# Kernel tuning notes

Measured on AMD Instinct MI355X. Metric: run time of the kernel, lower is better.

Reference implementation:

```python
import jax, jax.numpy as jnp
import numpy as np

NUM_HEADS = 16
D_MODEL = 1024
D_K = D_MODEL // NUM_HEADS
EPS = 1e-6


def setup_inputs() -> dict:
    key = jax.random.key(0)
    ks = jax.random.split(key, 12)
    B, S, D = 8, 1024, D_MODEL
    scale = 0.02
    return {
        "query": jax.random.normal(ks[0], (B, S, D), dtype=jnp.float32),
        "key": jax.random.normal(ks[1], (B, S, D), dtype=jnp.float32),
        "value": jax.random.normal(ks[2], (B, S, D), dtype=jnp.float32),
        "policy": jax.random.uniform(ks[3], (B, S, 1), dtype=jnp.float32),
        "wq_w": jax.random.normal(ks[4], (D, D), dtype=jnp.float32) * scale,
        "wq_b": jnp.zeros((D,), dtype=jnp.float32),
        "wk_w": jax.random.normal(ks[5], (D, D), dtype=jnp.float32) * scale,
        "wk_b": jnp.zeros((D,), dtype=jnp.float32),
        "wv_w": jax.random.normal(ks[6], (D, D), dtype=jnp.float32) * scale,
        "wv_b": jnp.zeros((D,), dtype=jnp.float32),
        "dense_w": jax.random.normal(ks[7], (D, D), dtype=jnp.float32) * scale,
        "dense_b": jnp.zeros((D,), dtype=jnp.float32),
    }


def _split_heads(x):
    B, S, D = x.shape
    return x.reshape(B, S, NUM_HEADS, D_K).transpose(0, 2, 1, 3)  # [B,H,S,dk]


def reference(query, key, value, policy, wq_w, wq_b, wk_w, wk_b, wv_w, wv_b, dense_w, dense_b):
    B, S, D = query.shape
    # torch Linear: y = x @ W.T + b
    q = _split_heads(query @ wq_w.T + wq_b)
    k = _split_heads(key @ wk_w.T + wk_b)
    v = _split_heads(value @ wv_w.T + wv_b)

    scores = jnp.einsum("bhqd,bhkd->bhqk", q, k) / jnp.sqrt(jnp.float32(D_K))
    # policy branch: exp * policy normalization (no softmax max-subtraction, faithful)
    attn_policy = policy.reshape(B, 1, 1, S)
    sc = jnp.exp(scores) * attn_policy
    p_attn = (sc + EPS / S) / (jnp.sum(sc, axis=-1, keepdims=True) + EPS)

    x = jnp.einsum("bhqk,bhkd->bhqd", p_attn, v)
    x = x.transpose(0, 2, 1, 3).reshape(B, S, D)
    out = x @ dense_w.T + dense_b  # dropout = identity (eval mode)
    return out
```

## Files before the change

kernel.cpp:

```cpp
#include <hip/hip_runtime.h>


#define Sdim 1024
#define Ddim 1024

typedef unsigned short u16;
typedef float f32x4 __attribute__((ext_vector_type(4)));
typedef float f32x16 __attribute__((ext_vector_type(16)));
typedef __bf16 bf16x8 __attribute__((ext_vector_type(8)));
typedef u16 u16x8 __attribute__((ext_vector_type(8)));
typedef unsigned u32x2 __attribute__((ext_vector_type(2)));
typedef __attribute__((address_space(3))) void lds_void;
typedef __attribute__((address_space(1))) void gbl_void;

__device__ __forceinline__ u16 f2bf(float f) {
    unsigned u = __float_as_uint(f);
    u += 0x7fffu + ((u >> 16) & 1u);
    return (u16)(u >> 16);
}
__device__ __forceinline__ void gld16(const void* g, void* l) {
    __builtin_amdgcn_global_load_lds((const gbl_void*)g, (lds_void*)l, 16, 0, 0);
}
__device__ __forceinline__ float fexp2(float x) {
#if __has_builtin(__builtin_amdgcn_exp2f)
    return __builtin_amdgcn_exp2f(x);
#else
    return __expf(x * 0.6931471805599453f);
#endif
}
__device__ __forceinline__ unsigned cvtpk(float lo, float hi) {
    unsigned r;
    asm("v_cvt_pk_bf16_f32 %0, %1, %2" : "=v"(r) : "v"(lo), "v"(hi));
    return r;
}
#define MFMA16(a, b, c) __builtin_amdgcn_mfma_f32_16x16x32_bf16((a), (b), (c), 0, 0, 0)
#define MFMA32(a, b, c) __builtin_amdgcn_mfma_f32_32x32x16_bf16((a), (b), (c), 0, 0, 0)
#define SCHEDB() __builtin_amdgcn_sched_barrier(0)

#define QSCALE 0.18033688011112042f

__global__ __launch_bounds__(256) void cvt_all(const float* __restrict__ s0,
                                               const float* __restrict__ s1,
                                               const float* __restrict__ s2,
                                               const float* __restrict__ s3,
                                               const float* __restrict__ s4,
                                               const float* __restrict__ s5,
                                               const float* __restrict__ s6,
                                               u16* __restrict__ d0, u16* __restrict__ d1,
                                               u16* __restrict__ d2, u16* __restrict__ d3,
                                               u16* __restrict__ d4, u16* __restrict__ d5,
                                               u16* __restrict__ d6) {
    const int z = blockIdx.y;
    if (z >= 3 && blockIdx.x >= 512) return;
    const float* s = z == 0 ? s0 : z == 1 ? s1 : z == 2 ? s2 : z == 3 ? s3
                   : z == 4 ? s4 : z == 5 ? s5 : s6;
    u16* d = z == 0 ? d0 : z == 1 ? d1 : z == 2 ? d2 : z == 3 ? d3
           : z == 4 ? d4 : z == 5 ? d5 : d6;
    const float sc = (z == 3) ? QSCALE : 1.0f;
    const int i = (blockIdx.x * 256 + threadIdx.x) * 8;
    const float4 a = *(const float4*)(s + i);
    const float4 b = *(const float4*)(s + i + 4);
    u16x8 o;
    o[0] = f2bf(a.x * sc); o[1] = f2bf(a.y * sc); o[2] = f2bf(a.z * sc); o[3] = f2bf(a.w * sc);
    o[4] = f2bf(b.x * sc); o[5] = f2bf(b.y * sc); o[6] = f2bf(b.z * sc); o[7] = f2bf(b.w * sc);
    *(u16x8*)(d + i) = o;
}

template <int OM>
__device__ __forceinline__ void gemm2p_body(const u16* __restrict__ A,
                                            const u16* __restrict__ W,
                                            const float* __restrict__ bias, float bscale,
                                            void* __restrict__ Cout,
                                            char* __restrict__ smem,
                                            int m0, int n0) {
    const int tid  = threadIdx.x;
    const int w    = tid >> 6;
    const int lane = tid & 63;
    const int l15  = lane & 15;
    const int quad = lane >> 4;
    const int wr   = w >> 1;
    const int wc   = w & 1;

    const int lrow = lane >> 3;
    const int scol = (((lane & 7) ^ lrow) << 3);
    const u16* pa = A + (size_t)(m0 + w * 32 + lrow) * Ddim + scol;
    const u16* pb = W + (size_t)(n0 + w * 16 + lrow) * Ddim + scol;
    char* sAw = smem + w * 4096;
    char* sBw = smem + 65536 + w * 2048;

#define STG(t, b)                                                             \
    do {                                                                      \
        const int k0 = (t) * 64;                                              \
        gld16(pa + k0,             sAw + (b) * 32768);                        \
        gld16(pa + k0 + 8 * 1024,  sAw + (b) * 32768 + 1024);                 \
        gld16(pa + k0 + 16 * 1024, sAw + (b) * 32768 + 2048);                 \
        gld16(pa + k0 + 24 * 1024, sAw + (b) * 32768 + 3072);                 \
        gld16(pb + k0,             sBw + (b) * 16384);                        \
        gld16(pb + k0 + 8 * 1024,  sBw + (b) * 16384 + 1024);                 \
    } while (0)

    const char* Ab = smem + (size_t)(wr * 64 + l15) * 128;
    const char* Bb = smem + 65536 + (size_t)(wc * 64 + l15) * 128;
    const int cx = ((quad ^ (l15 & 7)) << 4);

    f32x4 acc[4][4] = {};

    STG(0, 0);
    __syncthreads();

    for (int t = 0; t < 16; ++t) {
        const int boA = (t & 1) * 32768;
        const int boB = (t & 1) * 16384;
        if (t < 15) STG(t + 1, (t & 1) ^ 1);
        SCHEDB();
#pragma unroll
        for (int ks = 0; ks < 2; ++ks) {
            const int cxs = cx ^ (ks << 6);
            bf16x8 af[4], bfr[4];
#pragma unroll
            for (int i = 0; i < 4; ++i)
                af[i] = *(const bf16x8*)(Ab + boA + i * 2048 + cxs);
#pragma unroll
            for (int j = 0; j < 4; ++j)
                bfr[j] = *(const bf16x8*)(Bb + boB + j * 2048 + cxs);
#pragma unroll
            for (int i = 0; i < 4; ++i)
#pragma unroll
                for (int j = 0; j < 4; ++j)
                    acc[i][j] = MFMA16(af[i], bfr[j], acc[i][j]);
        }
        __syncthreads();
    }
#undef STG

    float bv[4];
#pragma unroll
    for (int j = 0; j < 4; ++j)
        bv[j] = bias[n0 + wc * 64 + j * 16 + l15] * bscale;

    if (OM == 2) {
        u16* Ts = (u16*)smem;
#pragma unroll
        for (int i = 0; i < 4; ++i)
#pragma unroll
            for (int j = 0; j < 4; ++j)
#pragma unroll
                for (int r = 0; r < 4; ++r)
                    Ts[(wr * 64 + i * 16 + quad * 4 + r) * 133 +
                       wc * 64 + j * 16 + l15] = f2bf(acc[i][j][r] + bv[j]);
        __syncthreads();
        const int dcol = tid >> 2;
        const int sp   = tid & 3;
        const int b    = m0 >> 10;
        const int sb0  = m0 & 1023;
        const int h    = (n0 >> 6) + (dcol >> 6);
        const int dd   = dcol & 63;
        u16* vrow = (u16*)Cout + ((size_t)((b << 4) + h) * 64 + dd) * Sdim + sb0;
#pragma unroll
        for (int sblk = 0; sblk < 4; ++sblk)
#pragma unroll
            for (int g = 0; g < 2; ++g) {
                const int c = sblk * 64 + sp * 16 + g * 8;
                u16x8 o;
#pragma unroll
                for (int e = 0; e < 8; ++e) o[e] = Ts[(c + e) * 133 + dcol];
                *(u16x8*)(vrow + c) = o;
            }
    } else {
#pragma unroll
        for (int i = 0; i < 4; ++i)
#pragma unroll
            for (int j = 0; j < 4; ++j)
#pragma unroll
                for (int r = 0; r < 4; ++r) {
                    const int row = m0 + wr * 64 + i * 16 + quad * 4 + r;
                    const int col = n0 + wc * 64 + j * 16 + l15;
                    const float v = acc[i][j][r] + bv[j];
                    if (OM == 1)
                        ((u16*)Cout)[(size_t)row * Ddim + col] = f2bf(v);
                    else
                        ((float*)Cout)[(size_t)row * Ddim + col] = v;
                }
    }
}

__global__ __launch_bounds__(512, 2) void gemm2p_qkv(
        const u16* __restrict__ A0, const u16* __restrict__ A1, const u16* __restrict__ A2,
        const u16* __restrict__ W0, const u16* __restrict__ W1, const u16* __restrict__ W2,
        const float* __restrict__ b0, const float* __restrict__ b1, const float* __restrict__ b2,
        u16* __restrict__ C0, u16* __restrict__ C1, u16* __restrict__ C2) {
    __shared__ __align__(16) char smem[98304];
    const int d = blockIdx.x;
    const int s = (d & 7) * 96 + (d >> 3);
    const int z = s >> 8;
    const int rr = s & 255;
    const int tm = rr >> 3, tn = rr & 7;
    const u16* A = z == 0 ? A0 : z == 1 ? A1 : A2;
    const u16* W = z == 0 ? W0 : z == 1 ? W1 : W2;
    const float* bias = z == 0 ? b0 : z == 1 ? b1 : b2;
    u16* C = z == 0 ? C0 : z == 1 ? C1 : C2;
    const float bsc = (z == 0) ? QSCALE : 1.0f;
    if (z == 2)
        gemm2p_body<2>(A, W, bias, bsc, (void*)C, smem, tm * 256, tn * 128);
    else
        gemm2p_body<1>(A, W, bias, bsc, (void*)C, smem, tm * 256, tn * 128);
}

__global__ __launch_bounds__(512, 2) void gemm2p_dense(const u16* __restrict__ A,
                                                       const u16* __restrict__ W,
                                                       const float* __restrict__ bias,
                                                       float* __restrict__ C) {
    __shared__ __align__(16) char smem[98304];
    const int d = blockIdx.x;
    const int s = (d & 7) * 32 + (d >> 3);
    const int tm = s >> 3, tn = s & 7;
    gemm2p_body<0>(A, W, bias, 1.0f, (void*)C, smem, tm * 256, tn * 128);
}

__global__ __launch_bounds__(256, 2) void attn_mfma(const u16* __restrict__ Qp,
                                                    const u16* __restrict__ Kp,
                                                    const u16* __restrict__ Vt,
                                                    const float* __restrict__ pol,
                                                    u16* __restrict__ Xb) {
    __shared__ __align__(16) u16 lds[37632];
    u16* Qs = lds;
    u16* Ks = lds + 18432;
    u16* Vs = lds + 27648;
    float* pols = (float*)(lds + 36864);
    float* denb = pols + 128;

    const int tid  = threadIdx.x;
    const int w    = tid >> 6;
    const int lane = tid & 63;
    const int l31  = lane & 31;
    const unsigned hsel = lane >> 5;
    const int bh = blockIdx.x;
    const int q0 = blockIdx.y * 256;
    const size_t bS = (size_t)(bh >> 4) * Sdim;
    const int col0 = (bh & 15) * 64;
    const int sr = tid >> 2;
    const int sc4 = tid & 3;

    const u16* Kg = Kp + (bS + sr) * Ddim + col0 + sc4 * 8;
    const u16* Vg = Vt + ((size_t)(bh * 64 + sr)) * Sdim + sc4 * 8;
    const float* pg = pol + bS + tid;

#pragma unroll
    for (int rg = 0; rg < 4; ++rg) {
        const int r = rg * 64 + sr;
#pragma unroll
        for (int g = 0; g < 2; ++g) {
            const int ch = sc4 + g * 4;
            *(u16x8*)(Qs + r * 72 + ch * 8) =
                *(const u16x8*)(Qp + (bS + q0 + r) * Ddim + col0 + ch * 8);
        }
    }
#pragma unroll
    for (int g = 0; g < 2; ++g) {
        *(u16x8*)(Ks + sr * 72 + (sc4 + g * 4) * 8) = *(const u16x8*)(Kg + g * 32);
        *(u16x8*)(Vs + sr * 72 + (sc4 + g * 4) * 8) = *(const u16x8*)(Vg + g * 32);
    }
    if (tid < 64) pols[tid] = pg[0];
    __syncthreads();

    bf16x8 Qf[2][4];
#pragma unroll
    for (int qt = 0; qt < 2; ++qt)
#pragma unroll
        for (int dkt = 0; dkt < 4; ++dkt)
            Qf[qt][dkt] = *(const bf16x8*)(Qs + (w * 64 + qt * 32 + l31) * 72 +
                                           dkt * 16 + hsel * 8);

    f32x16 X[2][2] = {};
    float den[2] = {0.f, 0.f};

    for (int kt = 0; kt < 16; ++kt) {
        const int cur = kt & 1;
        const bool pf = (kt < 15);
        u16x8 kr0 = {}, kr1 = {}, vr0 = {}, vr1 = {};
        float polr = 0.f;
        if (pf) {
            const int ko = (kt + 1) * 64;
            kr0 = *(const u16x8*)(Kg + (size_t)ko * Ddim);
            kr1 = *(const u16x8*)(Kg + (size_t)ko * Ddim + 32);
            vr0 = *(const u16x8*)(Vg + ko);
            vr1 = *(const u16x8*)(Vg + ko + 32);
            if (tid < 64) polr = pg[ko];
        }
        SCHEDB();

        const u16* Ksc = Ks + cur * 4608;
        const u16* Vsc = Vs + cur * 4608;
        const float* polc = pols + cur * 64;
#pragma unroll
        for (int t32 = 0; t32 < 2; ++t32) {
            float polv[16];
#pragma unroll
            for (int e = 0; e < 16; ++e)
                polv[e] = polc[t32 * 32 + (e & 3) + 8 * (e >> 2) + 4 * hsel];
            bf16x8 Kf[4];
#pragma unroll
            for (int dkt = 0; dkt < 4; ++dkt)
                Kf[dkt] = *(const bf16x8*)(Ksc + (t32 * 32 + l31) * 72 +
                                           dkt * 16 + hsel * 8);
#pragma unroll
            for (int qt = 0; qt < 2; ++qt) {
                f32x16 S = {};
#pragma unroll
                for (int dkt = 0; dkt < 4; ++dkt)
                    S = MFMA32(Kf[dkt], Qf[qt][dkt], S);
                float p[16];
#pragma unroll
                for (int e = 0; e < 16; ++e) {
                    p[e] = fexp2(S[e]) * polv[e];
                    den[qt] += p[e];
                }
                unsigned pk_[8];
#pragma unroll
                for (int g = 0; g < 4; ++g) {
                    pk_[2 * g]     = cvtpk(p[4 * g + 0], p[4 * g + 1]);
                    pk_[2 * g + 1] = cvtpk(p[4 * g + 2], p[4 * g + 3]);
                }
#pragma unroll
                for (int tau = 0; tau < 2; ++tau) {
                    const u32x2 sA = __builtin_amdgcn_permlane32_swap(
                        pk_[4 * tau + 0], pk_[4 * tau + 2], false, false);
                    const u32x2 sB = __builtin_amdgcn_permlane32_swap(
                        pk_[4 * tau + 1], pk_[4 * tau + 3], false, false);
                    union { unsigned u[4]; bf16x8 v; } Af;
                    Af.u[0] = sA[0]; Af.u[1] = sB[0];
                    Af.u[2] = sA[1]; Af.u[3] = sB[1];
#pragma unroll
                    for (int ndt = 0; ndt < 2; ++ndt) {
                        const bf16x8 Vf =
                            *(const bf16x8*)(Vsc + (ndt * 32 + l31) * 72 +
                                             t32 * 32 + tau * 16 + hsel * 8);
                        X[qt][ndt] = MFMA32(Af.v, Vf, X[qt][ndt]);
                    }
                }
            }
        }
        if (pf) {
            const int nxt = cur ^ 1;
            *(u16x8*)(Ks + nxt * 4608 + sr * 72 + sc4 * 8) = kr0;
            *(u16x8*)(Ks + nxt * 4608 + sr * 72 + (sc4 + 4) * 8) = kr1;
            *(u16x8*)(Vs + nxt * 4608 + sr * 72 + sc4 * 8) = vr0;
            *(u16x8*)(Vs + nxt * 4608 + sr * 72 + (sc4 + 4) * 8) = vr1;
            if (tid < 64) pols[nxt * 64 + tid] = polr;
        }
        __syncthreads();
    }

#pragma unroll
    for (int qt = 0; qt < 2; ++qt) {
        den[qt] += __shfl_xor(den[qt], 32);
        denb[w * 64 + qt * 32 + l31] = 1.0f / (den[qt] + 1e-6f);
    }
    u16* Xout = Qs;
#pragma unroll
    for (int qt = 0; qt < 2; ++qt) {
        float invv[16];
#pragma unroll
        for (int e = 0; e < 16; ++e)
            invv[e] = denb[w * 64 + qt * 32 + (e & 3) + 8 * (e >> 2) + 4 * hsel];
#pragma unroll
        for (int ndt = 0; ndt < 2; ++ndt)
#pragma unroll
            for (int e = 0; e < 16; ++e) {
                const int rho = (e & 3) + 8 * (e >> 2) + 4 * hsel;
                Xout[(w * 64 + qt * 32 + rho) * 72 + ndt * 32 + l31] =
                    f2bf(X[qt][ndt][e] * invv[e]);
            }
    }
    __syncthreads();
#pragma unroll
    for (int rg = 0; rg < 4; ++rg) {
        const int r = rg * 64 + sr;
#pragma unroll
        for (int g = 0; g < 2; ++g) {
            const int ch = sc4 + g * 4;
            *(u16x8*)(Xb + (bS + q0 + r) * Ddim + col0 + ch * 8) =
                *(const u16x8*)(Xout + r * 72 + ch * 8);
        }
    }
}

extern "C" void kernel_launch(void* const* d_in, const int* in_sizes, int n_in,
                              void* d_out, int out_size, void* d_ws, size_t ws_size,
                              hipStream_t stream) {
    const float* query   = (const float*)d_in[0];
    const float* key     = (const float*)d_in[1];
    const float* value   = (const float*)d_in[2];
    const float* policy  = (const float*)d_in[3];
    const float* wq_w    = (const float*)d_in[4];
    const float* wq_b    = (const float*)d_in[5];
    const float* wk_w    = (const float*)d_in[6];
    const float* wk_b    = (const float*)d_in[7];
    const float* wv_w    = (const float*)d_in[8];
    const float* wv_b    = (const float*)d_in[9];
    const float* dense_w = (const float*)d_in[10];
    const float* dense_b = (const float*)d_in[11];

    const size_t MM = 1u << 20;
    const size_t A8 = 8 * MM;
    u16* qa  = (u16*)d_ws;
    u16* ka  = qa + A8;
    u16* va  = ka + A8;
    u16* wqb = va + A8;
    u16* wkb = wqb + MM;
    u16* wvb = wkb + MM;
    u16* wdb = wvb + MM;
    u16* Qp  = wdb + MM;
    u16* Kp  = Qp + A8;
    u16* Vt  = Kp + A8;
    u16* Xb  = qa;

    cvt_all<<<dim3(4096, 7), 256, 0, stream>>>(query, key, value, wq_w, wk_w, wv_w, dense_w,
                                               qa, ka, va, wqb, wkb, wvb, wdb);

    gemm2p_qkv<<<dim3(768), 512, 0, stream>>>(qa, ka, va, wqb, wkb, wvb,
                                              wq_b, wk_b, wv_b, Qp, Kp, Vt);

    attn_mfma<<<dim3(128, 4), 256, 0, stream>>>(Qp, Kp, Vt, policy, Xb);

    gemm2p_dense<<<dim3(256), 512, 0, stream>>>(Xb, wdb, dense_b, (float*)d_out);
}
```

Measured before the change: 292.3 us.

## Fuse fp32-to-bf16 activation conversion into QKV GEMM A-tile staging

Removes the separate conversion pass over query/key/value. The QKV GEMM now loads fp32 activations into registers, converts them to packed bf16 and writes them to LDS after the MFMA loop of each K-step, so the global loads overlap compute. The weights are still converted by a smaller kernel. This saves the write and re-read of the bf16 activation copies, at the cost of more register pressure and VALU/LDS-store work inside the GEMM. Each A element is now read from global memory at 4 bytes once per N-tile.

```diff
diff --git a/kernel.cpp b/kernel.cpp
--- a/kernel.cpp
+++ b/kernel.cpp
@@ -10,6 +10,7 @@
 typedef __bf16 bf16x8 __attribute__((ext_vector_type(8)));
 typedef u16 u16x8 __attribute__((ext_vector_type(8)));
 typedef unsigned u32x2 __attribute__((ext_vector_type(2)));
+typedef unsigned u32x4 __attribute__((ext_vector_type(4)));
 typedef __attribute__((address_space(3))) void lds_void;
 typedef __attribute__((address_space(1))) void gbl_void;
 
@@ -39,24 +40,16 @@
 
 #define QSCALE 0.18033688011112042f
 
-__global__ __launch_bounds__(256) void cvt_all(const float* __restrict__ s0,
-                                               const float* __restrict__ s1,
-                                               const float* __restrict__ s2,
-                                               const float* __restrict__ s3,
-                                               const float* __restrict__ s4,
-                                               const float* __restrict__ s5,
-                                               const float* __restrict__ s6,
-                                               u16* __restrict__ d0, u16* __restrict__ d1,
-                                               u16* __restrict__ d2, u16* __restrict__ d3,
-                                               u16* __restrict__ d4, u16* __restrict__ d5,
-                                               u16* __restrict__ d6) {
+__global__ __launch_bounds__(256) void cvt_w(const float* __restrict__ s0,
+                                             const float* __restrict__ s1,
+                                             const float* __restrict__ s2,
+                                             const float* __restrict__ s3,
+                                             u16* __restrict__ d0, u16* __restrict__ d1,
+                                             u16* __restrict__ d2, u16* __restrict__ d3) {
     const int z = blockIdx.y;
-    if (z >= 3 && blockIdx.x >= 512) return;
-    const float* s = z == 0 ? s0 : z == 1 ? s1 : z == 2 ? s2 : z == 3 ? s3
-                   : z == 4 ? s4 : z == 5 ? s5 : s6;
-    u16* d = z == 0 ? d0 : z == 1 ? d1 : z == 2 ? d2 : z == 3 ? d3
-           : z == 4 ? d4 : z == 5 ? d5 : d6;
-    const float sc = (z == 3) ? QSCALE : 1.0f;
+    const float* s = z == 0 ? s0 : z == 1 ? s1 : z == 2 ? s2 : s3;
+    u16* d = z == 0 ? d0 : z == 1 ? d1 : z == 2 ? d2 : d3;
+    const float sc = (z == 0) ? QSCALE : 1.0f;
     const int i = (blockIdx.x * 256 + threadIdx.x) * 8;
     const float4 a = *(const float4*)(s + i);
     const float4 b = *(const float4*)(s + i + 4);
@@ -66,8 +59,8 @@
     *(u16x8*)(d + i) = o;
 }
 
-template <int OM>
-__device__ __forceinline__ void gemm2p_body(const u16* __restrict__ A,
+template <int OM, bool AF32>
+__device__ __forceinline__ void gemm2p_body(const void* __restrict__ Asrc,
                                             const u16* __restrict__ W,
                                             const float* __restrict__ bias, float bscale,
                                             void* __restrict__ Cout,
@@ -83,20 +76,49 @@
 
     const int lrow = lane >> 3;
     const int scol = (((lane & 7) ^ lrow) << 3);
-    const u16* pa = A + (size_t)(m0 + w * 32 + lrow) * Ddim + scol;
+    const u16*   pa  = AF32 ? nullptr
+                            : (const u16*)Asrc + (size_t)(m0 + w * 32 + lrow) * Ddim + scol;
+    const float* paf = AF32 ? (const float*)Asrc + (size_t)(m0 + w * 32 + lrow) * Ddim + scol
+                            : nullptr;
     const u16* pb = W + (size_t)(n0 + w * 16 + lrow) * Ddim + scol;
     char* sAw = smem + w * 4096;
+    char* sAd = sAw + lane * 16;
     char* sBw = smem + 65536 + w * 2048;
 
-#define STG(t, b)                                                             \
+#define STG_A16(t, b)                                                         \
     do {                                                                      \
         const int k0 = (t) * 64;                                              \
         gld16(pa + k0,             sAw + (b) * 32768);                        \
         gld16(pa + k0 + 8 * 1024,  sAw + (b) * 32768 + 1024);                 \
         gld16(pa + k0 + 16 * 1024, sAw + (b) * 32768 + 2048);                 \
         gld16(pa + k0 + 24 * 1024, sAw + (b) * 32768 + 3072);                 \
-        gld16(pb + k0,             sBw + (b) * 16384);                        \
-        gld16(pb + k0 + 8 * 1024,  sBw + (b) * 16384 + 1024);                 \
+    } while (0)
+#define LDF(t, r0, r1)                                                        \
+    do {                                                                      \
+        const float* pt_ = paf + (t) * 64;                                    \
+        _Pragma("unroll")                                                     \
+        for (int j_ = 0; j_ < 4; ++j_) {                                      \
+            r0[j_] = *(const float4*)(pt_ + j_ * 8192);                       \
+            r1[j_] = *(const float4*)(pt_ + j_ * 8192 + 4);                   \
+        }                                                                     \
+    } while (0)
+#define WRF(b, r0, r1)                                                        \
+    do {                                                                      \
+        _Pragma("unroll")                                                     \
+        for (int j_ = 0; j_ < 4; ++j_) {                                      \
+            u32x4 o_;                                                         \
+            o_[0] = cvtpk(r0[j_].x, r0[j_].y);                                \
+            o_[1] = cvtpk(r0[j_].z, r0[j_].w);                                \
+            o_[2] = cvtpk(r1[j_].x, r1[j_].y);                                \
+            o_[3] = cvtpk(r1[j_].z, r1[j_].w);                                \
+            *(u32x4*)(sAd + (b) * 32768 + j_ * 1024) = o_;                    \
+        }                                                                     \
+    } while (0)
+#define STG_B(t, b)                                                           \
+    do {                                                                      \
+        const int k0 = (t) * 64;                                              \
+        gld16(pb + k0,            sBw + (b) * 16384);                         \
+        gld16(pb + k0 + 8 * 1024, sBw + (b) * 16384 + 1024);                  \
     } while (0)
 
     const char* Ab = smem + (size_t)(wr * 64 + l15) * 128;
@@ -105,13 +127,26 @@
 
     f32x4 acc[4][4] = {};
 
-    STG(0, 0);
+    if (AF32) {
+        float4 p0[4], p1[4];
+        LDF(0, p0, p1);
+        WRF(0, p0, p1);
+    } else {
+        STG_A16(0, 0);
+    }
+    STG_B(0, 0);
     __syncthreads();
 
     for (int t = 0; t < 16; ++t) {
         const int boA = (t & 1) * 32768;
         const int boB = (t & 1) * 16384;
-        if (t < 15) STG(t + 1, (t & 1) ^ 1);
+        const int nb = (t & 1) ^ 1;
+        float4 r0[4], r1[4];
+        if (t < 15) {
+            if (AF32) LDF(t + 1, r0, r1);
+            else      STG_A16(t + 1, nb);
+            STG_B(t + 1, nb);
+        }
         SCHEDB();
 #pragma unroll
         for (int ks = 0; ks < 2; ++ks) {
@@ -129,9 +164,13 @@
                 for (int j = 0; j < 4; ++j)
                     acc[i][j] = MFMA16(af[i], bfr[j], acc[i][j]);
         }
+        if (AF32 && t < 15) WRF(nb, r0, r1);
         __syncthreads();
     }
-#undef STG
+#undef STG_A16
+#undef LDF
+#undef WRF
+#undef STG_B
 
     float bv[4];
 #pragma unroll
@@ -185,7 +224,7 @@
 }
 
 __global__ __launch_bounds__(512, 2) void gemm2p_qkv(
-        const u16* __restrict__ A0, const u16* __restrict__ A1, const u16* __restrict__ A2,
+        const float* __restrict__ A0, const float* __restrict__ A1, const float* __restrict__ A2,
         const u16* __restrict__ W0, const u16* __restrict__ W1, const u16* __restrict__ W2,
         const float* __restrict__ b0, const float* __restrict__ b1, const float* __restrict__ b2,
         u16* __restrict__ C0, u16* __restrict__ C1, u16* __restrict__ C2) {
@@ -195,15 +234,15 @@
     const int z = s >> 8;
     const int rr = s & 255;
     const int tm = rr >> 3, tn = rr & 7;
-    const u16* A = z == 0 ? A0 : z == 1 ? A1 : A2;
+    const float* A = z == 0 ? A0 : z == 1 ? A1 : A2;
     const u16* W = z == 0 ? W0 : z == 1 ? W1 : W2;
     const float* bias = z == 0 ? b0 : z == 1 ? b1 : b2;
     u16* C = z == 0 ? C0 : z == 1 ? C1 : C2;
     const float bsc = (z == 0) ? QSCALE : 1.0f;
     if (z == 2)
-        gemm2p_body<2>(A, W, bias, bsc, (void*)C, smem, tm * 256, tn * 128);
+        gemm2p_body<2, true>(A, W, bias, bsc, (void*)C, smem, tm * 256, tn * 128);
     else
-        gemm2p_body<1>(A, W, bias, bsc, (void*)C, smem, tm * 256, tn * 128);
+        gemm2p_body<1, true>(A, W, bias, bsc, (void*)C, smem, tm * 256, tn * 128);
 }
 
 __global__ __launch_bounds__(512, 2) void gemm2p_dense(const u16* __restrict__ A,
@@ -214,7 +253,7 @@
     const int d = blockIdx.x;
     const int s = (d & 7) * 32 + (d >> 3);
     const int tm = s >> 3, tn = s & 7;
-    gemm2p_body<0>(A, W, bias, 1.0f, (void*)C, smem, tm * 256, tn * 128);
+    gemm2p_body<0, false>(A, W, bias, 1.0f, (void*)C, smem, tm * 256, tn * 128);
 }
 
 __global__ __launch_bounds__(256, 2) void attn_mfma(const u16* __restrict__ Qp,
@@ -403,22 +442,19 @@
 
     const size_t MM = 1u << 20;
     const size_t A8 = 8 * MM;
-    u16* qa  = (u16*)d_ws;
-    u16* ka  = qa + A8;
-    u16* va  = ka + A8;
-    u16* wqb = va + A8;
+    u16* Xb  = (u16*)d_ws;
+    u16* wqb = Xb + A8;
     u16* wkb = wqb + MM;
     u16* wvb = wkb + MM;
     u16* wdb = wvb + MM;
     u16* Qp  = wdb + MM;
     u16* Kp  = Qp + A8;
     u16* Vt  = Kp + A8;
-    u16* Xb  = qa;
-
-    cvt_all<<<dim3(4096, 7), 256, 0, stream>>>(query, key, value, wq_w, wk_w, wv_w, dense_w,
-                                               qa, ka, va, wqb, wkb, wvb, wdb);
-
-    gemm2p_qkv<<<dim3(768), 512, 0, stream>>>(qa, ka, va, wqb, wkb, wvb,
+
+    cvt_w<<<dim3(512, 4), 256, 0, stream>>>(wq_w, wk_w, wv_w, dense_w,
+                                            wqb, wkb, wvb, wdb);
+
+    gemm2p_qkv<<<dim3(768), 512, 0, stream>>>(query, key, value, wqb, wkb, wvb,
                                               wq_b, wk_b, wv_b, Qp, Kp, Vt);
 
     attn_mfma<<<dim3(128, 4), 256, 0, stream>>>(Qp, Kp, Vt, policy, Xb);
```

New measurement: 325.8 us. +11.5%, slower.
